# Optimization experiments

Hardware: AMD Instinct MI355X
Metric: run time of the kernel (lower is better)

The kernel has to match this reference:

```python
import jax, jax.numpy as jnp
import numpy as np

N = 50000      # nodes
E = 400000     # edges (before self-loops)
IN = 128       # input feature dim
HID = 32       # out_channels per head
HEADS = 12
NC = 2         # num_classes
SLOPE = 0.2    # GATv2 leaky_relu negative slope


def setup_inputs() -> dict:
    key = jax.random.key(0)
    ks = jax.random.split(key, 24)
    f32 = jnp.float32
    def nrm(k, shape, s=0.1):
        return jax.random.normal(k, shape, dtype=f32) * s
    inp = {}
    inp["x"] = jax.random.normal(ks[0], (N, IN), dtype=f32)
    inp["edge_index"] = jax.random.randint(ks[1], (2, E), 0, N, dtype=jnp.int32)
    # GATv2 layer 0: in=IN, layer 1: in=HID; both heads=HEADS, out=HID, concat=False
    dims = [IN, HID]
    i = 2
    for l, d in enumerate(dims):
        inp[f"Wl{l}"] = nrm(ks[i], (d, HEADS * HID)); i += 1
        inp[f"bl{l}"] = jnp.zeros((HEADS * HID,), f32)
        inp[f"Wr{l}"] = nrm(ks[i], (d, HEADS * HID)); i += 1
        inp[f"br{l}"] = jnp.zeros((HEADS * HID,), f32)
        inp[f"att{l}"] = nrm(ks[i], (HEADS, HID)); i += 1
        inp[f"bias{l}"] = jnp.zeros((HID,), f32)
    # output GATv2Conv(HID, NC): heads=1, concat=True
    inp["Wlo"] = nrm(ks[i], (HID, NC)); i += 1
    inp["blo"] = jnp.zeros((NC,), f32)
    inp["Wro"] = nrm(ks[i], (HID, NC)); i += 1
    inp["bro"] = jnp.zeros((NC,), f32)
    inp["atto"] = nrm(ks[i], (1, NC)); i += 1
    inp["biaso"] = jnp.zeros((NC,), f32)
    return inp


def gatv2_conv(x, src, dst, Wl, bl, Wr, br, att, bias, heads, out_ch, concat):
    """PyG GATv2Conv (share_weights=False, self-loops pre-appended, eval mode)."""
    n = x.shape[0]
    xl = (x @ Wl + bl).reshape(n, heads, out_ch)   # source transform
    xr = (x @ Wr + br).reshape(n, heads, out_ch)   # target transform
    # per-edge attention: e_ij = att . leaky_relu(xl_j + xr_i)
    h = jax.nn.leaky_relu(xl[src] + xr[dst], SLOPE)            # [E, H, C]
    logits = jnp.einsum('ehc,hc->eh', h, att)                   # [E, H]
    # segment softmax over incoming edges per destination node
    m = jax.ops.segment_max(logits, dst, num_segments=n)        # [N, H]
    a = jnp.exp(logits - m[dst])
    denom = jax.ops.segment_sum(a, dst, num_segments=n)         # [N, H]
    alpha = a / (denom[dst] + 1e-16)                            # [E, H]
    out = jax.ops.segment_sum(xl[src] * alpha[..., None], dst, num_segments=n)
    out = out.reshape(n, heads * out_ch) if concat else out.mean(axis=1)
    return out + bias


def reference(x, edge_index, Wl0, bl0, Wr0, br0, att0, bias0,
              Wl1, bl1, Wr1, br1, att1, bias1,
              Wlo, blo, Wro, bro, atto, biaso):
    n = x.shape[0]
    loop = jnp.arange(n, dtype=edge_index.dtype)
    src = jnp.concatenate([edge_index[0], loop])  # add self-loops (PyG default)
    dst = jnp.concatenate([edge_index[1], loop])
    h = gatv2_conv(x, src, dst, Wl0, bl0, Wr0, br0, att0, bias0, HEADS, HID, False)
    h = jax.nn.elu(h)
    h = gatv2_conv(h, src, dst, Wl1, bl1, Wr1, br1, att1, bias1, HEADS, HID, False)
    h = jax.nn.elu(h)
    out = gatv2_conv(h, src, dst, Wlo, blo, Wro, bro, atto, biaso, 1, NC, True)
    return out
```

## Files before the change

kernel.cpp:

```cpp
#include <hip/hip_runtime.h>
#include <hip/hip_fp16.h>
#include <math.h>

#define IN_DIM 128
#define HID 32
#define HEADS 12
#define FDIM (HEADS*HID)
#define SLOPE 0.2f

typedef __attribute__((ext_vector_type(8))) short short8;
typedef __attribute__((ext_vector_type(4))) float float4v;
typedef __attribute__((ext_vector_type(4))) float f32x4;
typedef _Float16 hv2 __attribute__((ext_vector_type(2)));

__device__ __forceinline__ float dot2acc(hv2 a, hv2 b, float c) {
#if __has_builtin(__builtin_amdgcn_fdot2)
    return __builtin_amdgcn_fdot2(a, b, c, false);
#else
    return c + (float)a.x * (float)b.x + (float)a.y * (float)b.y;
#endif
}


__global__ void hist_kernel(const int* __restrict__ dst, int* __restrict__ cnt, int E) {
    int e = blockIdx.x * blockDim.x + threadIdx.x;
    if (e < E) atomicAdd(&cnt[dst[e]], 1);
}

__global__ __launch_bounds__(256) void scan_partial_kernel(const int* __restrict__ cnt,
                                                           int* __restrict__ partials, int n) {
    int i = blockIdx.x * 256 + threadIdx.x;
    int v = (i < n) ? cnt[i] : 0;
#pragma unroll
    for (int off = 1; off < 64; off <<= 1) v += __shfl_xor(v, off);
    __shared__ int sh[4];
    if ((threadIdx.x & 63) == 0) sh[threadIdx.x >> 6] = v;
    __syncthreads();
    if (threadIdx.x == 0) partials[blockIdx.x] = sh[0] + sh[1] + sh[2] + sh[3];
}

__global__ __launch_bounds__(1024) void scan_top_kernel(int* __restrict__ partials, int nb) {
    __shared__ int sh[1024];
    int t = threadIdx.x;
    int v = (t < nb) ? partials[t] : 0;
    sh[t] = v;
    __syncthreads();
    for (int off = 1; off < 1024; off <<= 1) {
        int u = (t >= off) ? sh[t - off] : 0;
        __syncthreads();
        sh[t] += u;
        __syncthreads();
    }
    if (t < nb) partials[t] = sh[t] - v;
}

__global__ __launch_bounds__(256) void scan_final_kernel(const int* __restrict__ cnt,
                                                         const int* __restrict__ partials,
                                                         int* __restrict__ start,
                                                         int* __restrict__ cursor, int n) {
    __shared__ int sh[256];
    int t = threadIdx.x;
    int i = blockIdx.x * 256 + t;
    int v = (i < n) ? cnt[i] : 0;
    sh[t] = v;
    __syncthreads();
    for (int off = 1; off < 256; off <<= 1) {
        int u = (t >= off) ? sh[t - off] : 0;
        __syncthreads();
        sh[t] += u;
        __syncthreads();
    }
    int ex = sh[t] - v + partials[blockIdx.x];
    if (i < n) {
        start[i] = ex;
        cursor[i] = ex;
        if (i == n - 1) start[n] = ex + v;
    }
}

__global__ void scatter_kernel(const int* __restrict__ src, const int* __restrict__ dst,
                               int* __restrict__ cursor, int* __restrict__ srcs,
                               int* __restrict__ srcsOff, int E) {
    int e = blockIdx.x * blockDim.x + threadIdx.x;
    if (e < E) {
        int d = dst[e];
        int pos = atomicAdd(&cursor[d], 1);
        int s = src[e];
        srcs[pos] = s;
        srcsOff[pos] = s * (FDIM * 2);
    }
}


__device__ __forceinline__ unsigned int bf16_rne(float f) {
    unsigned int u = __float_as_uint(f);
    return (u + 0x7FFFu + ((u >> 16) & 1u)) >> 16;
}


__global__ void prep_all(const float* __restrict__ Wl0, const float* __restrict__ Wr0,
                         const float* __restrict__ Wl1, const float* __restrict__ Wr1,
                         const float* __restrict__ a0, const float* __restrict__ a1,
                         short* __restrict__ Bl0h, short* __restrict__ Bl0l,
                         short* __restrict__ Br0h, short* __restrict__ Br0l,
                         short* __restrict__ Bl1h, short* __restrict__ Bl1l,
                         short* __restrict__ Br1h, short* __restrict__ Br1l,
                         _Float16* __restrict__ attH) {
    int idx = blockIdx.x * 256 + threadIdx.x;
    if (idx < 49152) {
        int k = idx / 384, n = idx - k * 384;
        float w1 = Wl0[idx], w2 = Wr0[idx];
        unsigned int h1 = bf16_rne(w1);
        unsigned int l1 = bf16_rne(w1 - __uint_as_float(h1 << 16));
        unsigned int h2 = bf16_rne(w2);
        unsigned int l2 = bf16_rne(w2 - __uint_as_float(h2 << 16));
        Bl0h[n * 128 + k] = (short)h1;  Bl0l[n * 128 + k] = (short)l1;
        Br0h[n * 128 + k] = (short)h2;  Br0l[n * 128 + k] = (short)l2;
    } else if (idx < 61440) {
        int i2 = idx - 49152;
        int k = i2 / 384, n = i2 - k * 384;
        float w1 = Wl1[i2], w2 = Wr1[i2];
        unsigned int h1 = bf16_rne(w1);
        unsigned int l1 = bf16_rne(w1 - __uint_as_float(h1 << 16));
        unsigned int h2 = bf16_rne(w2);
        unsigned int l2 = bf16_rne(w2 - __uint_as_float(h2 << 16));
        Bl1h[n * 32 + k] = (short)h1;  Bl1l[n * 32 + k] = (short)l1;
        Br1h[n * 32 + k] = (short)h2;  Br1l[n * 32 + k] = (short)l2;
    } else if (idx < 62208) {
        int i2 = idx - 61440;
        attH[i2] = (_Float16)((i2 < 384) ? a0[i2] : a1[i2 - 384]);
    }
}


__global__ __launch_bounds__(256) void gemm_pair_mfma_f32A(
    const float* __restrict__ A,
    const short* __restrict__ B1h, const short* __restrict__ B1l,
    const float* __restrict__ bias1, __half* __restrict__ C1,
    const short* __restrict__ B2h, const short* __restrict__ B2l,
    const float* __restrict__ bias2, __half* __restrict__ C2,
    int M, int K) {
    __shared__ __align__(16) unsigned char smem[33792];
    uint4* AsHi = (uint4*)smem;
    uint4* AsLo = AsHi + 512;
    uint4* BsHi = AsLo + 512;
    uint4* BsLo = BsHi + 512;
    int tid = threadIdx.x;
    int lane = tid & 63;
    int wave = tid >> 6;
    int wm = wave & 1, wn = wave >> 1;
    int rowBase = blockIdx.x * 128;
    bool second = blockIdx.y >= 3;
    int colBase = (blockIdx.y - (second ? 3 : 0)) * 128;
    const short* Bh  = second ? B2h : B1h;
    const short* Bl  = second ? B2l : B1l;
    const float* bias = second ? bias2 : bias1;
    __half*      C    = second ? C2 : C1;

    float4v acc[4][4];
#pragma unroll
    for (int i = 0; i < 4; i++)
#pragma unroll
        for (int j = 0; j < 4; j++) acc[i][j] = (float4v){0.f, 0.f, 0.f, 0.f};

    for (int kt = 0; kt < K; kt += 32) {
#pragma unroll
        for (int i = 0; i < 2; i++) {
            int c = i * 256 + tid;
            int o = c >> 7, r = c & 127;
            int gr = rowBase + r;
            float4 f0 = make_float4(0.f, 0.f, 0.f, 0.f), f1 = f0;
            if (gr < M) {
                const float* p = A + (size_t)gr * K + kt + o * 8;
                f0 = *(const float4*)p;
                f1 = *(const float4*)(p + 4);
            }
            float fs[8] = {f0.x, f0.y, f0.z, f0.w, f1.x, f1.y, f1.z, f1.w};
            unsigned int hb[8], lb[8];
#pragma unroll
            for (int t = 0; t < 8; t++) {
                hb[t] = bf16_rne(fs[t]);
                lb[t] = bf16_rne(fs[t] - __uint_as_float(hb[t] << 16));
            }
            uint4 hi, lo;
            hi.x = hb[0] | (hb[1] << 16); hi.y = hb[2] | (hb[3] << 16);
            hi.z = hb[4] | (hb[5] << 16); hi.w = hb[6] | (hb[7] << 16);
            lo.x = lb[0] | (lb[1] << 16); lo.y = lb[2] | (lb[3] << 16);
            lo.z = lb[4] | (lb[5] << 16); lo.w = lb[6] | (lb[7] << 16);
            int slot = (r >> 4) * 64 + (o << 4) + (r & 15);
            AsHi[slot] = hi;
            AsLo[slot] = lo;
        }
#pragma unroll
        for (int i = 0; i < 4; i++) {
            int c = i * 256 + tid;
            int h = c >> 9, o = (c >> 7) & 3, n = c & 127;
            const short* src = h ? Bl : Bh;
            uint4 v = *(const uint4*)(src + (size_t)(colBase + n) * K + kt + o * 8);
            int slot = (n >> 4) * 64 + (o << 4) + (n & 15);
            if (h) BsLo[slot] = v; else BsHi[slot] = v;
        }
        __syncthreads();

        short8 ah[4], al[4], bh[4], blv[4];
#pragma unroll
        for (int i = 0; i < 4; i++) {
            ah[i]  = ((const short8*)AsHi)[(wm * 4 + i) * 64 + lane];
            al[i]  = ((const short8*)AsLo)[(wm * 4 + i) * 64 + lane];
            bh[i]  = ((const short8*)BsHi)[(wn * 4 + i) * 64 + lane];
            blv[i] = ((const short8*)BsLo)[(wn * 4 + i) * 64 + lane];
        }
#pragma unroll
        for (int i = 0; i < 4; i++)
#pragma unroll
            for (int j = 0; j < 4; j++) {
                acc[i][j] = __builtin_amdgcn_mfma_f32_16x16x32_bf16(ah[i], bh[j],  acc[i][j], 0, 0, 0);
                acc[i][j] = __builtin_amdgcn_mfma_f32_16x16x32_bf16(ah[i], blv[j], acc[i][j], 0, 0, 0);
                acc[i][j] = __builtin_amdgcn_mfma_f32_16x16x32_bf16(al[i], bh[j],  acc[i][j], 0, 0, 0);
            }
        __syncthreads();
    }

    float* Ct = (float*)smem;
    int cq = lane >> 4, cn = lane & 15;
#pragma unroll
    for (int ph = 0; ph < 2; ph++) {
        if (wm == ph) {
#pragma unroll
            for (int i = 0; i < 4; i++)
#pragma unroll
                for (int j = 0; j < 4; j++) {
                    int lr = i * 16 + cq * 4;
                    int lc = wn * 64 + j * 16 + cn;
#pragma unroll
                    for (int r = 0; r < 4; r++)
                        Ct[(lr + r) * 132 + lc] = acc[i][j][r];
                }
        }
        __syncthreads();
#pragma unroll
        for (int k = 0; k < 4; k++) {
            int o = k * 256 + tid;
            int lr = o >> 4;
            int oc = (o & 15) << 3;
            int gr = rowBase + ph * 64 + lr;
            if (gr < M) {
                float4 f0 = *(float4*)&Ct[lr * 132 + oc];
                float4 f1 = *(float4*)&Ct[lr * 132 + oc + 4];
                int gc = colBase + oc;
                float4 b0 = *(const float4*)(bias + gc);
                float4 b1 = *(const float4*)(bias + gc + 4);
                __half2 p0 = __floats2half2_rn(f0.x + b0.x, f0.y + b0.y);
                __half2 p1 = __floats2half2_rn(f0.z + b0.z, f0.w + b0.w);
                __half2 p2 = __floats2half2_rn(f1.x + b1.x, f1.y + b1.y);
                __half2 p3 = __floats2half2_rn(f1.z + b1.z, f1.w + b1.w);
                uint4 ov;
                ov.x = *(unsigned int*)&p0;
                ov.y = *(unsigned int*)&p1;
                ov.z = *(unsigned int*)&p2;
                ov.w = *(unsigned int*)&p3;
                *(uint4*)(C + (size_t)gr * FDIM + gc) = ov;
            }
        }
        __syncthreads();
    }
}


__global__ __launch_bounds__(256) void gemm_pair_mfma_preA(
    const short* __restrict__ Ahi, const short* __restrict__ Alo,
    const short* __restrict__ B1h, const short* __restrict__ B1l,
    const float* __restrict__ bias1, __half* __restrict__ C1,
    const short* __restrict__ B2h, const short* __restrict__ B2l,
    const float* __restrict__ bias2, __half* __restrict__ C2,
    int M, int K) {
    __shared__ __align__(16) unsigned char smem[33792];
    uint4* AsHi = (uint4*)smem;
    uint4* AsLo = AsHi + 512;
    uint4* BsHi = AsLo + 512;
    uint4* BsLo = BsHi + 512;
    int tid = threadIdx.x;
    int lane = tid & 63;
    int wave = tid >> 6;
    int wm = wave & 1, wn = wave >> 1;
    int rowBase = blockIdx.x * 128;
    bool second = blockIdx.y >= 3;
    int colBase = (blockIdx.y - (second ? 3 : 0)) * 128;
    const short* Bh  = second ? B2h : B1h;
    const short* Bl  = second ? B2l : B1l;
    const float* bias = second ? bias2 : bias1;
    __half*      C    = second ? C2 : C1;

    float4v acc[4][4];
#pragma unroll
    for (int i = 0; i < 4; i++)
#pragma unroll
        for (int j = 0; j < 4; j++) acc[i][j] = (float4v){0.f, 0.f, 0.f, 0.f};

    for (int kt = 0; kt < K; kt += 32) {
#pragma unroll
        for (int i = 0; i < 2; i++) {
            int c = i * 256 + tid;
            int o = c >> 7, r = c & 127;
            int gr = rowBase + r;
            uint4 hv = make_uint4(0, 0, 0, 0), lv = hv;
            if (gr < M) {
                hv = *(const uint4*)(Ahi + (size_t)gr * K + kt + o * 8);
                lv = *(const uint4*)(Alo + (size_t)gr * K + kt + o * 8);
            }
            int slot = (r >> 4) * 64 + (o << 4) + (r & 15);
            AsHi[slot] = hv;
            AsLo[slot] = lv;
        }
#pragma unroll
        for (int i = 0; i < 4; i++) {
            int c = i * 256 + tid;
            int h = c >> 9, o = (c >> 7) & 3, n = c & 127;
            const short* src = h ? Bl : Bh;
            uint4 v = *(const uint4*)(src + (size_t)(colBase + n) * K + kt + o * 8);
            int slot = (n >> 4) * 64 + (o << 4) + (n & 15);
            if (h) BsLo[slot] = v; else BsHi[slot] = v;
        }
        __syncthreads();

        short8 ah[4], al[4], bh[4], blv[4];
#pragma unroll
        for (int i = 0; i < 4; i++) {
            ah[i]  = ((const short8*)AsHi)[(wm * 4 + i) * 64 + lane];
            al[i]  = ((const short8*)AsLo)[(wm * 4 + i) * 64 + lane];
            bh[i]  = ((const short8*)BsHi)[(wn * 4 + i) * 64 + lane];
            blv[i] = ((const short8*)BsLo)[(wn * 4 + i) * 64 + lane];
        }
#pragma unroll
        for (int i = 0; i < 4; i++)
#pragma unroll
            for (int j = 0; j < 4; j++) {
                acc[i][j] = __builtin_amdgcn_mfma_f32_16x16x32_bf16(ah[i], bh[j],  acc[i][j], 0, 0, 0);
                acc[i][j] = __builtin_amdgcn_mfma_f32_16x16x32_bf16(ah[i], blv[j], acc[i][j], 0, 0, 0);
                acc[i][j] = __builtin_amdgcn_mfma_f32_16x16x32_bf16(al[i], bh[j],  acc[i][j], 0, 0, 0);
            }
        __syncthreads();
    }

    float* Ct = (float*)smem;
    int cq = lane >> 4, cn = lane & 15;
#pragma unroll
    for (int ph = 0; ph < 2; ph++) {
        if (wm == ph) {
#pragma unroll
            for (int i = 0; i < 4; i++)
#pragma unroll
                for (int j = 0; j < 4; j++) {
                    int lr = i * 16 + cq * 4;
                    int lc = wn * 64 + j * 16 + cn;
#pragma unroll
                    for (int r = 0; r < 4; r++)
                        Ct[(lr + r) * 132 + lc] = acc[i][j][r];
                }
        }
        __syncthreads();
#pragma unroll
        for (int k = 0; k < 4; k++) {
            int o = k * 256 + tid;
            int lr = o >> 4;
            int oc = (o & 15) << 3;
            int gr = rowBase + ph * 64 + lr;
            if (gr < M) {
                float4 f0 = *(float4*)&Ct[lr * 132 + oc];
                float4 f1 = *(float4*)&Ct[lr * 132 + oc + 4];
                int gc = colBase + oc;
                float4 b0 = *(const float4*)(bias + gc);
                float4 b1 = *(const float4*)(bias + gc + 4);
                __half2 p0 = __floats2half2_rn(f0.x + b0.x, f0.y + b0.y);
                __half2 p1 = __floats2half2_rn(f0.z + b0.z, f0.w + b0.w);
                __half2 p2 = __floats2half2_rn(f1.x + b1.x, f1.y + b1.y);
                __half2 p3 = __floats2half2_rn(f1.z + b1.z, f1.w + b1.w);
                uint4 ov;
                ov.x = *(unsigned int*)&p0;
                ov.y = *(unsigned int*)&p1;
                ov.z = *(unsigned int*)&p2;
                ov.w = *(unsigned int*)&p3;
                *(uint4*)(C + (size_t)gr * FDIM + gc) = ov;
            }
        }
        __syncthreads();
    }
}


__global__ __launch_bounds__(64) void agg_kernel(const __half* __restrict__ xl,
                                                 const __half* __restrict__ xr,
                                                 const _Float16* __restrict__ att_h,
                                                 const float* __restrict__ bias,
                                                 const int* __restrict__ start,
                                                 const int* __restrict__ srcsOff,
                                                 short* __restrict__ houtHi,
                                                 short* __restrict__ houtLo,
                                                 const float* __restrict__ Wl,
                                                 const float* __restrict__ bl,
                                                 const float* __restrict__ Wr,
                                                 const float* __restrict__ br,
                                                 float* __restrict__ xloB,
                                                 float* __restrict__ xroB, int N) {
    int node = blockIdx.x;
    if (node >= N) return;
    int lane = threadIdx.x & 63;
    int hl = lane & 31;
    int half_ = lane >> 5;
    int cb = hl << 3;

    long nodeOff = (long)node * (FDIM * 2);
    hv2 xr2[6], at2[6];
    f32x4 acc[3];
    float s[3];
#pragma unroll
    for (int c = 0; c < 3; c++) {
        uint2 ur = *(const uint2*)((const char*)xr + nodeOff + c * 256 + cb);
        xr2[2*c]   = __builtin_bit_cast(hv2, ur.x);
        xr2[2*c+1] = __builtin_bit_cast(hv2, ur.y);
        uint2 ua = *(const uint2*)((const char*)att_h + c * 256 + cb);
        at2[2*c]   = __builtin_bit_cast(hv2, ua.x);
        at2[2*c+1] = __builtin_bit_cast(hv2, ua.y);
        acc[c] = (f32x4){0.f, 0.f, 0.f, 0.f};
        s[c] = 0.f;
    }
    const hv2 sl2 = {(_Float16)SLOPE, (_Float16)SLOPE};
    const char* xlb = (const char*)xl;

    int e0 = start[node], e1 = start[node + 1];

    for (int b = e0 - 1; b < e1; b += 4) {
        hv2 xa[2][6];
        float mask[2];
#pragma unroll
        for (int p = 0; p < 2; p++) {
            int myIdx = b + p * 2 + half_;
            int ic = min(myIdx, e1 - 1);
            long off = (ic < e0) ? nodeOff : (long)srcsOff[ic];
            mask[p] = (myIdx < e1) ? 0.f : -1e30f;
            const char* base = xlb + off + cb;
            uint2 u0 = *(const uint2*)(base);
            uint2 u1 = *(const uint2*)(base + 256);
            uint2 u2 = *(const uint2*)(base + 512);
            xa[p][0] = __builtin_bit_cast(hv2, u0.x); xa[p][1] = __builtin_bit_cast(hv2, u0.y);
            xa[p][2] = __builtin_bit_cast(hv2, u1.x); xa[p][3] = __builtin_bit_cast(hv2, u1.y);
            xa[p][4] = __builtin_bit_cast(hv2, u2.x); xa[p][5] = __builtin_bit_cast(hv2, u2.y);
        }
#pragma unroll
        for (int p = 0; p < 2; p++) {
            float pc[3];
#pragma unroll
            for (int c = 0; c < 3; c++) {
                hv2 t0 = xa[p][2*c]   + xr2[2*c];
                hv2 t1 = xa[p][2*c+1] + xr2[2*c+1];
                t0 = __builtin_elementwise_max(t0, t0 * sl2);
                t1 = __builtin_elementwise_max(t1, t1 * sl2);
                pc[c] = dot2acc(t1, at2[2*c+1], dot2acc(t0, at2[2*c], 0.f));
            }
#pragma unroll
            for (int st = 1; st <= 4; st <<= 1) {
                pc[0] += __shfl_xor(pc[0], st);
                pc[1] += __shfl_xor(pc[1], st);
                pc[2] += __shfl_xor(pc[2], st);
            }
#pragma unroll
            for (int c = 0; c < 3; c++) {
                float a = __expf(pc[c] + mask[p]);
                s[c] += a;
                acc[c].x = fmaf(a, (float)xa[p][2*c].x,   acc[c].x);
                acc[c].y = fmaf(a, (float)xa[p][2*c].y,   acc[c].y);
                acc[c].z = fmaf(a, (float)xa[p][2*c+1].x, acc[c].z);
                acc[c].w = fmaf(a, (float)xa[p][2*c+1].y, acc[c].w);
            }
        }
    }

#pragma unroll
    for (int c = 0; c < 3; c++) {
        acc[c].x += __shfl_xor(acc[c].x, 32);
        acc[c].y += __shfl_xor(acc[c].y, 32);
        acc[c].z += __shfl_xor(acc[c].z, 32);
        acc[c].w += __shfl_xor(acc[c].w, 32);
        s[c] += __shfl_xor(s[c], 32);
    }
    f32x4 v[3];
#pragma unroll
    for (int c = 0; c < 3; c++) {
        float inv = 1.f / (s[c] + 1e-16f);
        f32x4 iv = {inv, inv, inv, inv};
        v[c] = acc[c] * iv;
    }
#pragma unroll
    for (int st = 8; st <= 16; st <<= 1) {
#pragma unroll
        for (int c = 0; c < 3; c++) {
            v[c].x += __shfl_xor(v[c].x, st);
            v[c].y += __shfl_xor(v[c].y, st);
            v[c].z += __shfl_xor(v[c].z, st);
            v[c].w += __shfl_xor(v[c].w, st);
        }
    }
    if (lane < 8) {
        f32x4 b4 = *(const f32x4*)(bias + (hl << 2));
        f32x4 o = (v[0] + v[1] + v[2]) * (f32x4){1.f/12.f, 1.f/12.f, 1.f/12.f, 1.f/12.f} + b4;
        o.x = o.x > 0.f ? o.x : expm1f(o.x);
        o.y = o.y > 0.f ? o.y : expm1f(o.y);
        o.z = o.z > 0.f ? o.z : expm1f(o.z);
        o.w = o.w > 0.f ? o.w : expm1f(o.w);
        if (houtHi) {
            float fs[4] = {o.x, o.y, o.z, o.w};
            unsigned int hb[4], lb[4];
#pragma unroll
            for (int t = 0; t < 4; t++) {
                hb[t] = bf16_rne(fs[t]);
                lb[t] = bf16_rne(fs[t] - __uint_as_float(hb[t] << 16));
            }
            uint2 hp, lp;
            hp.x = hb[0] | (hb[1] << 16); hp.y = hb[2] | (hb[3] << 16);
            lp.x = lb[0] | (lb[1] << 16); lp.y = lb[2] | (lb[3] << 16);
            *(uint2*)(houtHi + (size_t)node * 32 + (hl << 2)) = hp;
            *(uint2*)(houtLo + (size_t)node * 32 + (hl << 2)) = lp;
        }
        if (Wl) {
            f32x4 wl0 = *(const f32x4*)(Wl + (hl << 3));
            f32x4 wl1 = *(const f32x4*)(Wl + (hl << 3) + 4);
            f32x4 wr0 = *(const f32x4*)(Wr + (hl << 3));
            f32x4 wr1 = *(const f32x4*)(Wr + (hl << 3) + 4);
            float l0 = o.x * wl0.x + o.y * wl0.z + o.z * wl1.x + o.w * wl1.z;
            float l1 = o.x * wl0.y + o.y * wl0.w + o.z * wl1.y + o.w * wl1.w;
            float r0 = o.x * wr0.x + o.y * wr0.z + o.z * wr1.x + o.w * wr1.z;
            float r1 = o.x * wr0.y + o.y * wr0.w + o.z * wr1.y + o.w * wr1.w;
#pragma unroll
            for (int st = 1; st <= 4; st <<= 1) {
                l0 += __shfl_xor(l0, st); l1 += __shfl_xor(l1, st);
                r0 += __shfl_xor(r0, st); r1 += __shfl_xor(r1, st);
            }
            if (hl == 0) {
                xloB[2 * node]     = l0 + bl[0];
                xloB[2 * node + 1] = l1 + bl[1];
                xroB[2 * node]     = r0 + br[0];
                xroB[2 * node + 1] = r1 + br[1];
            }
        }
    }
}


__global__ void out_agg_kernel(const float* __restrict__ xlo, const float* __restrict__ xro,
                               const float* __restrict__ atto, const float* __restrict__ biaso,
                               const int* __restrict__ start, const int* __restrict__ srcs,
                               float* __restrict__ out, int N) {
    int i = blockIdx.x * blockDim.x + threadIdx.x;
    if (i >= N) return;
    float a0 = atto[0], a1 = atto[1];
    float xr0 = xro[2 * i], xr1 = xro[2 * i + 1];
    float s = 0.f, acc0 = 0.f, acc1 = 0.f;
    int e0 = start[i], e1 = start[i + 1];
    for (int idx = e0 - 1; idx < e1; ++idx) {
        int j = (idx < e0) ? i : srcs[idx];
        float x0 = xlo[2 * j], x1 = xlo[2 * j + 1];
        float t0 = x0 + xr0, t1 = x1 + xr1;
        t0 = fmaxf(t0, SLOPE * t0);
        t1 = fmaxf(t1, SLOPE * t1);
        float L = a0 * t0 + a1 * t1;
        float a = __expf(L);
        s += a;
        acc0 = fmaf(a, x0, acc0);
        acc1 = fmaf(a, x1, acc1);
    }
    float inv = 1.0f / (s + 1e-16f);
    out[2 * i]     = acc0 * inv + biaso[0];
    out[2 * i + 1] = acc1 * inv + biaso[1];
}


extern "C" void kernel_launch(void* const* d_in, const int* in_sizes, int n_in,
                              void* d_out, int out_size, void* d_ws, size_t ws_size,
                              hipStream_t stream) {
    const float* x    = (const float*)d_in[0];
    const int*   ei   = (const int*)d_in[1];
    const float* Wl0  = (const float*)d_in[2];
    const float* bl0  = (const float*)d_in[3];
    const float* Wr0  = (const float*)d_in[4];
    const float* br0  = (const float*)d_in[5];
    const float* att0 = (const float*)d_in[6];
    const float* bias0= (const float*)d_in[7];
    const float* Wl1  = (const float*)d_in[8];
    const float* bl1  = (const float*)d_in[9];
    const float* Wr1  = (const float*)d_in[10];
    const float* br1  = (const float*)d_in[11];
    const float* att1 = (const float*)d_in[12];
    const float* bias1= (const float*)d_in[13];
    const float* Wlo  = (const float*)d_in[14];
    const float* blo  = (const float*)d_in[15];
    const float* Wro  = (const float*)d_in[16];
    const float* bro  = (const float*)d_in[17];
    const float* atto = (const float*)d_in[18];
    const float* biaso= (const float*)d_in[19];

    const int N = in_sizes[0] / IN_DIM;
    const int E = in_sizes[1] / 2;

    char* ws = (char*)d_ws;
    size_t off = 0;
    auto take = [&](size_t bytes) -> char* {
        char* p = ws + off;
        off += (bytes + 255) & ~(size_t)255;
        return p;
    };
    __half* xlf = (__half*)take((size_t)N * FDIM * 2);
    __half* xrf = (__half*)take((size_t)N * FDIM * 2);
    float* xloB = (float*)take((size_t)N * 2 * 4);
    float* xroB = (float*)take((size_t)N * 2 * 4);
    int* cnt    = (int*)take((size_t)N * 4);
    int* startA = (int*)take((size_t)(N + 1) * 4);
    int* cursor = (int*)take((size_t)N * 4);
    int* srcs   = (int*)take((size_t)E * 4);
    int* srcsOff= (int*)take((size_t)E * 4);
    int  nb     = (N + 255) / 256;
    int* partials = (int*)take((size_t)nb * 4);
    short* Bl0h = (short*)take((size_t)FDIM * IN_DIM * 2);
    short* Bl0l = (short*)take((size_t)FDIM * IN_DIM * 2);
    short* Br0h = (short*)take((size_t)FDIM * IN_DIM * 2);
    short* Br0l = (short*)take((size_t)FDIM * IN_DIM * 2);
    short* Bl1h = (short*)take((size_t)FDIM * HID * 2);
    short* Bl1l = (short*)take((size_t)FDIM * HID * 2);
    short* Br1h = (short*)take((size_t)FDIM * HID * 2);
    short* Br1l = (short*)take((size_t)FDIM * HID * 2);
    short* h0h  = (short*)take((size_t)N * HID * 2);
    short* h0l  = (short*)take((size_t)N * HID * 2);
    _Float16* attH = (_Float16*)take((size_t)768 * 2);

    const int* esrc = ei;
    const int* edst = ei + E;

    prep_all<<<(62208 + 255) / 256, 256, 0, stream>>>(Wl0, Wr0, Wl1, Wr1, att0, att1,
                                                      Bl0h, Bl0l, Br0h, Br0l,
                                                      Bl1h, Bl1l, Br1h, Br1l, attH);

    hipMemsetAsync(cnt, 0, (size_t)N * 4, stream);
    hist_kernel<<<(E + 255) / 256, 256, 0, stream>>>(edst, cnt, E);
    scan_partial_kernel<<<nb, 256, 0, stream>>>(cnt, partials, N);
    scan_top_kernel<<<1, 1024, 0, stream>>>(partials, nb);
    scan_final_kernel<<<nb, 256, 0, stream>>>(cnt, partials, startA, cursor, N);
    scatter_kernel<<<(E + 255) / 256, 256, 0, stream>>>(esrc, edst, cursor, srcs, srcsOff, E);

    dim3 ggrid((N + 127) / 128, 6);
    gemm_pair_mfma_f32A<<<ggrid, 256, 0, stream>>>(x, Bl0h, Bl0l, bl0, xlf, Br0h, Br0l, br0, xrf, N, IN_DIM);
    agg_kernel<<<N, 64, 0, stream>>>(xlf, xrf, attH, bias0, startA, srcsOff,
                                     h0h, h0l, nullptr, nullptr, nullptr, nullptr,
                                     nullptr, nullptr, N);
    gemm_pair_mfma_preA<<<ggrid, 256, 0, stream>>>(h0h, h0l, Bl1h, Bl1l, bl1, xlf, Br1h, Br1l, br1, xrf, N, HID);
    agg_kernel<<<N, 64, 0, stream>>>(xlf, xrf, attH + 384, bias1, startA, srcsOff,
                                     nullptr, nullptr, Wlo, blo, Wro, bro,
                                     xloB, xroB, N);
    out_agg_kernel<<<(N + 255) / 256, 256, 0, stream>>>(xloB, xroB, atto, biaso, startA, srcs, (float*)d_out, N);
}
```

Measured before the change: 390.4 us.

## Pre-split x to bf16 hi/lo and load MFMA fragments directly from global

Adds a separate kernel that splits x into bf16 high/low planes once, replacing the in-GEMM fp32-to-bf16 conversion. Both GEMMs now share one kernel that loads MFMA operand fragments straight from global memory into registers, dropping the LDS staging and the per-k-tile barriers. LDS is kept only for the epilogue transpose. The trade-off is an extra pass over x plus scratch buffers, and uncoalesced strided global reads with no bounds check on rows past M (N is not a multiple of 128). The extra 16 KB scratch allocation appears meant to keep those overrunning reads in bounds.

```diff
diff --git a/kernel.cpp b/kernel.cpp
--- a/kernel.cpp
+++ b/kernel.cpp
@@ -133,18 +133,34 @@
 }
 
 
-__global__ __launch_bounds__(256) void gemm_pair_mfma_f32A(
-    const float* __restrict__ A,
+__global__ void conv_x_kernel(const float* __restrict__ A, short* __restrict__ Ah,
+                              short* __restrict__ Al, int total4) {
+    int i = blockIdx.x * 256 + threadIdx.x;
+    if (i >= total4) return;
+    float4 v = ((const float4*)A)[i];
+    float fs[4] = {v.x, v.y, v.z, v.w};
+    unsigned int hb[4], lb[4];
+#pragma unroll
+    for (int t = 0; t < 4; t++) {
+        hb[t] = bf16_rne(fs[t]);
+        lb[t] = bf16_rne(fs[t] - __uint_as_float(hb[t] << 16));
+    }
+    uint2 hp, lp;
+    hp.x = hb[0] | (hb[1] << 16); hp.y = hb[2] | (hb[3] << 16);
+    lp.x = lb[0] | (lb[1] << 16); lp.y = lb[2] | (lb[3] << 16);
+    ((uint2*)Ah)[i] = hp;
+    ((uint2*)Al)[i] = lp;
+}
+
+
+__global__ __launch_bounds__(256) void gemm_pair_direct(
+    const short* __restrict__ Ahi, const short* __restrict__ Alo,
     const short* __restrict__ B1h, const short* __restrict__ B1l,
     const float* __restrict__ bias1, __half* __restrict__ C1,
     const short* __restrict__ B2h, const short* __restrict__ B2l,
     const float* __restrict__ bias2, __half* __restrict__ C2,
     int M, int K) {
-    __shared__ __align__(16) unsigned char smem[33792];
-    uint4* AsHi = (uint4*)smem;
-    uint4* AsLo = AsHi + 512;
-    uint4* BsHi = AsLo + 512;
-    uint4* BsLo = BsHi + 512;
+    __shared__ __align__(16) float Ct[64 * 132];
     int tid = threadIdx.x;
     int lane = tid & 63;
     int wave = tid >> 6;
@@ -157,58 +173,29 @@
     const float* bias = second ? bias2 : bias1;
     __half*      C    = second ? C2 : C1;
 
+    int fr = lane & 15;
+    int fo = (lane >> 4) << 3;
+
     float4v acc[4][4];
 #pragma unroll
     for (int i = 0; i < 4; i++)
 #pragma unroll
         for (int j = 0; j < 4; j++) acc[i][j] = (float4v){0.f, 0.f, 0.f, 0.f};
 
+    const short* Ar = Ahi + (long)(rowBase + wm * 64 + fr) * K + fo;
+    const short* Al_ = Alo + (long)(rowBase + wm * 64 + fr) * K + fo;
+    const short* Br_ = Bh + (long)(colBase + wn * 64 + fr) * K + fo;
+    const short* Bl_ = Bl + (long)(colBase + wn * 64 + fr) * K + fo;
+    long rstep = (long)16 * K;
+
     for (int kt = 0; kt < K; kt += 32) {
-#pragma unroll
-        for (int i = 0; i < 2; i++) {
-            int c = i * 256 + tid;
-            int o = c >> 7, r = c & 127;
-            int gr = rowBase + r;
-            float4 f0 = make_float4(0.f, 0.f, 0.f, 0.f), f1 = f0;
-            if (gr < M) {
-                const float* p = A + (size_t)gr * K + kt + o * 8;
-                f0 = *(const float4*)p;
-                f1 = *(const float4*)(p + 4);
-            }
-            float fs[8] = {f0.x, f0.y, f0.z, f0.w, f1.x, f1.y, f1.z, f1.w};
-            unsigned int hb[8], lb[8];
-#pragma unroll
-            for (int t = 0; t < 8; t++) {
-                hb[t] = bf16_rne(fs[t]);
-                lb[t] = bf16_rne(fs[t] - __uint_as_float(hb[t] << 16));
-            }
-            uint4 hi, lo;
-            hi.x = hb[0] | (hb[1] << 16); hi.y = hb[2] | (hb[3] << 16);
-            hi.z = hb[4] | (hb[5] << 16); hi.w = hb[6] | (hb[7] << 16);
-            lo.x = lb[0] | (lb[1] << 16); lo.y = lb[2] | (lb[3] << 16);
-            lo.z = lb[4] | (lb[5] << 16); lo.w = lb[6] | (lb[7] << 16);
-            int slot = (r >> 4) * 64 + (o << 4) + (r & 15);
-            AsHi[slot] = hi;
-            AsLo[slot] = lo;
-        }
+        short8 ah[4], al[4], bh[4], blv[4];
 #pragma unroll
         for (int i = 0; i < 4; i++) {
-            int c = i * 256 + tid;
-            int h = c >> 9, o = (c >> 7) & 3, n = c & 127;
-            const short* src = h ? Bl : Bh;
-            uint4 v = *(const uint4*)(src + (size_t)(colBase + n) * K + kt + o * 8);
-            int slot = (n >> 4) * 64 + (o << 4) + (n & 15);
-            if (h) BsLo[slot] = v; else BsHi[slot] = v;
-        }
-        __syncthreads();
-
-        short8 ah[4], al[4], bh[4], blv[4];
-#pragma unroll
-        for (int i = 0; i < 4; i++) {
-            ah[i]  = ((const short8*)AsHi)[(wm * 4 + i) * 64 + lane];
-            al[i]  = ((const short8*)AsLo)[(wm * 4 + i) * 64 + lane];
-            bh[i]  = ((const short8*)BsHi)[(wn * 4 + i) * 64 + lane];
-            blv[i] = ((const short8*)BsLo)[(wn * 4 + i) * 64 + lane];
+            ah[i]  = *(const short8*)(Ar  + i * rstep + kt);
+            al[i]  = *(const short8*)(Al_ + i * rstep + kt);
+            bh[i]  = *(const short8*)(Br_ + i * rstep + kt);
+            blv[i] = *(const short8*)(Bl_ + i * rstep + kt);
         }
 #pragma unroll
         for (int i = 0; i < 4; i++)
@@ -218,13 +205,12 @@
                 acc[i][j] = __builtin_amdgcn_mfma_f32_16x16x32_bf16(ah[i], blv[j], acc[i][j], 0, 0, 0);
                 acc[i][j] = __builtin_amdgcn_mfma_f32_16x16x32_bf16(al[i], bh[j],  acc[i][j], 0, 0, 0);
             }
+    }
+
+    int cq = lane >> 4, cn = lane & 15;
+#pragma unroll
+    for (int ph = 0; ph < 2; ph++) {
         __syncthreads();
-    }
-
-    float* Ct = (float*)smem;
-    int cq = lane >> 4, cn = lane & 15;
-#pragma unroll
-    for (int ph = 0; ph < 2; ph++) {
         if (wm == ph) {
 #pragma unroll
             for (int i = 0; i < 4; i++)
@@ -262,128 +248,6 @@
                 *(uint4*)(C + (size_t)gr * FDIM + gc) = ov;
             }
         }
-        __syncthreads();
-    }
-}
-
-
-__global__ __launch_bounds__(256) void gemm_pair_mfma_preA(
-    const short* __restrict__ Ahi, const short* __restrict__ Alo,
-    const short* __restrict__ B1h, const short* __restrict__ B1l,
-    const float* __restrict__ bias1, __half* __restrict__ C1,
-    const short* __restrict__ B2h, const short* __restrict__ B2l,
-    const float* __restrict__ bias2, __half* __restrict__ C2,
-    int M, int K) {
-    __shared__ __align__(16) unsigned char smem[33792];
-    uint4* AsHi = (uint4*)smem;
-    uint4* AsLo = AsHi + 512;
-    uint4* BsHi = AsLo + 512;
-    uint4* BsLo = BsHi + 512;
-    int tid = threadIdx.x;
-    int lane = tid & 63;
-    int wave = tid >> 6;
-    int wm = wave & 1, wn = wave >> 1;
-    int rowBase = blockIdx.x * 128;
-    bool second = blockIdx.y >= 3;
-    int colBase = (blockIdx.y - (second ? 3 : 0)) * 128;
-    const short* Bh  = second ? B2h : B1h;
-    const short* Bl  = second ? B2l : B1l;
-    const float* bias = second ? bias2 : bias1;
-    __half*      C    = second ? C2 : C1;
-
-    float4v acc[4][4];
-#pragma unroll
-    for (int i = 0; i < 4; i++)
-#pragma unroll
-        for (int j = 0; j < 4; j++) acc[i][j] = (float4v){0.f, 0.f, 0.f, 0.f};
-
-    for (int kt = 0; kt < K; kt += 32) {
-#pragma unroll
-        for (int i = 0; i < 2; i++) {
-            int c = i * 256 + tid;
-            int o = c >> 7, r = c & 127;
-            int gr = rowBase + r;
-            uint4 hv = make_uint4(0, 0, 0, 0), lv = hv;
-            if (gr < M) {
-                hv = *(const uint4*)(Ahi + (size_t)gr * K + kt + o * 8);
-                lv = *(const uint4*)(Alo + (size_t)gr * K + kt + o * 8);
-            }
-            int slot = (r >> 4) * 64 + (o << 4) + (r & 15);
-            AsHi[slot] = hv;
-            AsLo[slot] = lv;
-        }
-#pragma unroll
-        for (int i = 0; i < 4; i++) {
-            int c = i * 256 + tid;
-            int h = c >> 9, o = (c >> 7) & 3, n = c & 127;
-            const short* src = h ? Bl : Bh;
-            uint4 v = *(const uint4*)(src + (size_t)(colBase + n) * K + kt + o * 8);
-            int slot = (n >> 4) * 64 + (o << 4) + (n & 15);
-            if (h) BsLo[slot] = v; else BsHi[slot] = v;
-        }
-        __syncthreads();
-
-        short8 ah[4], al[4], bh[4], blv[4];
-#pragma unroll
-        for (int i = 0; i < 4; i++) {
-            ah[i]  = ((const short8*)AsHi)[(wm * 4 + i) * 64 + lane];
-            al[i]  = ((const short8*)AsLo)[(wm * 4 + i) * 64 + lane];
-            bh[i]  = ((const short8*)BsHi)[(wn * 4 + i) * 64 + lane];
-            blv[i] = ((const short8*)BsLo)[(wn * 4 + i) * 64 + lane];
-        }
-#pragma unroll
-        for (int i = 0; i < 4; i++)
-#pragma unroll
-            for (int j = 0; j < 4; j++) {
-                acc[i][j] = __builtin_amdgcn_mfma_f32_16x16x32_bf16(ah[i], bh[j],  acc[i][j], 0, 0, 0);
-                acc[i][j] = __builtin_amdgcn_mfma_f32_16x16x32_bf16(ah[i], blv[j], acc[i][j], 0, 0, 0);
-                acc[i][j] = __builtin_amdgcn_mfma_f32_16x16x32_bf16(al[i], bh[j],  acc[i][j], 0, 0, 0);
-            }
-        __syncthreads();
-    }
-
-    float* Ct = (float*)smem;
-    int cq = lane >> 4, cn = lane & 15;
-#pragma unroll
-    for (int ph = 0; ph < 2; ph++) {
-        if (wm == ph) {
-#pragma unroll
-            for (int i = 0; i < 4; i++)
-#pragma unroll
-                for (int j = 0; j < 4; j++) {
-                    int lr = i * 16 + cq * 4;
-                    int lc = wn * 64 + j * 16 + cn;
-#pragma unroll
-                    for (int r = 0; r < 4; r++)
-                        Ct[(lr + r) * 132 + lc] = acc[i][j][r];
-                }
-        }
-        __syncthreads();
-#pragma unroll
-        for (int k = 0; k < 4; k++) {
-            int o = k * 256 + tid;
-            int lr = o >> 4;
-            int oc = (o & 15) << 3;
-            int gr = rowBase + ph * 64 + lr;
-            if (gr < M) {
-                float4 f0 = *(float4*)&Ct[lr * 132 + oc];
-                float4 f1 = *(float4*)&Ct[lr * 132 + oc + 4];
-                int gc = colBase + oc;
-                float4 b0 = *(const float4*)(bias + gc);
-                float4 b1 = *(const float4*)(bias + gc + 4);
-                __half2 p0 = __floats2half2_rn(f0.x + b0.x, f0.y + b0.y);
-                __half2 p1 = __floats2half2_rn(f0.z + b0.z, f0.w + b0.w);
-                __half2 p2 = __floats2half2_rn(f1.x + b1.x, f1.y + b1.y);
-                __half2 p3 = __floats2half2_rn(f1.z + b1.z, f1.w + b1.w);
-                uint4 ov;
-                ov.x = *(unsigned int*)&p0;
-                ov.y = *(unsigned int*)&p1;
-                ov.z = *(unsigned int*)&p2;
-                ov.w = *(unsigned int*)&p3;
-                *(uint4*)(C + (size_t)gr * FDIM + gc) = ov;
-            }
-        }
-        __syncthreads();
     }
 }
 
@@ -627,9 +491,12 @@
     short* Bl1l = (short*)take((size_t)FDIM * HID * 2);
     short* Br1h = (short*)take((size_t)FDIM * HID * 2);
     short* Br1l = (short*)take((size_t)FDIM * HID * 2);
+    short* xh   = (short*)take((size_t)N * IN_DIM * 2);
+    short* xlo_ = (short*)take((size_t)N * IN_DIM * 2);
     short* h0h  = (short*)take((size_t)N * HID * 2);
     short* h0l  = (short*)take((size_t)N * HID * 2);
     _Float16* attH = (_Float16*)take((size_t)768 * 2);
+    (void)take(16384);
 
     const int* esrc = ei;
     const int* edst = ei + E;
@@ -637,6 +504,7 @@
     prep_all<<<(62208 + 255) / 256, 256, 0, stream>>>(Wl0, Wr0, Wl1, Wr1, att0, att1,
                                                       Bl0h, Bl0l, Br0h, Br0l,
                                                       Bl1h, Bl1l, Br1h, Br1l, attH);
+    conv_x_kernel<<<((N * IN_DIM / 4) + 255) / 256, 256, 0, stream>>>(x, xh, xlo_, N * IN_DIM / 4);
 
     hipMemsetAsync(cnt, 0, (size_t)N * 4, stream);
     hist_kernel<<<(E + 255) / 256, 256, 0, stream>>>(edst, cnt, E);
@@ -646,11 +514,11 @@
     scatter_kernel<<<(E + 255) / 256, 256, 0, stream>>>(esrc, edst, cursor, srcs, srcsOff, E);
 
     dim3 ggrid((N + 127) / 128, 6);
-    gemm_pair_mfma_f32A<<<ggrid, 256, 0, stream>>>(x, Bl0h, Bl0l, bl0, xlf, Br0h, Br0l, br0, xrf, N, IN_DIM);
+    gemm_pair_direct<<<ggrid, 256, 0, stream>>>(xh, xlo_, Bl0h, Bl0l, bl0, xlf, Br0h, Br0l, br0, xrf, N, IN_DIM);
     agg_kernel<<<N, 64, 0, stream>>>(xlf, xrf, attH, bias0, startA, srcsOff,
                                      h0h, h0l, nullptr, nullptr, nullptr, nullptr,
                                      nullptr, nullptr, N);
-    gemm_pair_mfma_preA<<<ggrid, 256, 0, stream>>>(h0h, h0l, Bl1h, Bl1l, bl1, xlf, Br1h, Br1l, br1, xrf, N, HID);
+    gemm_pair_direct<<<ggrid, 256, 0, stream>>>(h0h, h0l, Bl1h, Bl1l, bl1, xlf, Br1h, Br1l, br1, xrf, N, HID);
     agg_kernel<<<N, 64, 0, stream>>>(xlf, xrf, attH + 384, bias1, startA, srcsOff,
                                      nullptr, nullptr, Wlo, blo, Wro, bro,
                                      xloB, xroB, N);
```

Measured after the change: 422.1 us. 1.08x slower.
